# Kernel optimization log

Measured on AMD Instinct MI355X. Metric: run time of the kernel, lower is better.

## Reference

```python
import jax, jax.numpy as jnp
import numpy as np

VEC_DIM = 64
RANK = 2


def setup_inputs() -> dict:
    key = jax.random.key(0)
    kg, km, kp = jax.random.split(key, 3)
    grid = jax.random.normal(kg, (193, 193, VEC_DIM), dtype=jnp.float32)
    # nn.init.uniform_(M.weight, -0.5, 0.5)
    M_weight = jax.random.uniform(km, (VEC_DIM, VEC_DIM), minval=-0.5, maxval=0.5, dtype=jnp.float32)
    # nn.init.uniform_(P, -0.1, 0.1)
    P = jax.random.uniform(kp, (VEC_DIM, VEC_DIM), minval=-0.1, maxval=0.1, dtype=jnp.float32)
    return {"grid": grid, "M_weight": M_weight, "P": P}


def reference(grid, M_weight, P):
    H, W, m = grid.shape
    # periods1[i,j] = periods2[i,j] = i*m + j + 2
    periods = (jnp.arange(m, dtype=jnp.float32)[:, None] * m
               + jnp.arange(m, dtype=jnp.float32)[None, :] + 2.0)  # [m, m]

    # ---- window extraction: linear mode (step=1), rank_mode='drop', rank_op='avg' ----
    nH = H - RANK + 1
    nW = W - RANK + 1
    win_sum = jax.lax.reduce_window(grid, 0.0, jax.lax.add,
                                    (RANK, RANK, 1), (1, 1, 1), 'VALID')  # [nH, nW, m]
    x_win = (win_sum / float(RANK * RANK)).reshape(nH * nW, m)  # [B, m]

    # ---- map through M (nn.Linear, no bias): y = x @ W^T ----
    x = x_win @ M_weight.T  # [B, m]

    # ---- phi_table gather: phi[k1,k2] = cos(2*pi*k1/periods) * cos(2*pi*k2/periods) ----
    two_pi = jnp.float32(2.0 * np.pi)
    k1s = jnp.arange(nH, dtype=jnp.float32)
    k2s = jnp.arange(nW, dtype=jnp.float32)
    cos1 = jnp.cos(two_pi * k1s[:, None, None] / periods)  # [nH, m, m]
    cos2 = jnp.cos(two_pi * k2s[:, None, None] / periods)  # [nW, m, m]
    phi = (cos1[:, None, :, :] * cos2[None, :, :, :]).reshape(nH * nW, m, m)  # [B, m, m]

    # ---- Nk = einsum('bj,ij,bij->bi', x, P, phi) ----
    Nk = jnp.einsum('bj,ij,bij->bi', x, P, phi)  # [B, m]
    return Nk
```

## Files before the change

### kernel.cpp

```cpp
#include <hip/hip_runtime.h>
#include <math.h>

#define NH 192
#define NW 192
#define Wt 193
#define TG 24
#define NTILE (TG*TG)
#define TILE_SZ 4096
#define TBLK 3072

__device__ __forceinline__ float cos_rev(float num, float den) {
    float rev = num * __builtin_amdgcn_rcpf(den);
    rev = __builtin_amdgcn_fractf(rev);
    return __builtin_amdgcn_cosf(rev);
}

__global__ __launch_bounds__(256) void k_prep(const float* __restrict__ grid,
                                              const float* __restrict__ Mw,
                                              const float* __restrict__ P,
                                              float* __restrict__ Cz,
                                              float* __restrict__ CP1,
                                              float* __restrict__ xt) {
    __shared__ float Ms[64 * 64];
    __shared__ float win[64 * 68];
    int bx = blockIdx.x;
    int t = threadIdx.x;

    if (bx < TBLK) {
        int idx = bx * 256 + t;
        int r  = idx & 3;
        int i  = (idx >> 2) & 63;
        int kg = (idx >> 8) % 48;
        int j  = idx / 12288;
        int k  = kg * 4 + r;
        Cz[idx] = cos_rev((float)k, (float)(i * 64 + j + 2));
        int i2 = idx & 63;
        int k2 = (idx >> 6) % 192;
        int j2 = idx / 12288;
        int t2 = i2 * 64 + j2;
        CP1[idx] = cos_rev((float)k2, (float)(t2 + 2)) * P[t2];
        return;
    }

    int bb = bx - TBLK;
    int k1g = bb % TG, k2g = bb / TG;

    #pragma unroll
    for (int r = 0; r < 4; ++r) {
        int e = r * 256 + t;
        ((float4*)Ms)[e] = ((const float4*)Mw)[e];
    }

    {
        int c = t & 63, pq = t >> 6;
        const float* gb = grid + ((size_t)(k1g * 8) * Wt + k2g * 8) * 64;
        #pragma unroll
        for (int r = 0; r < 16; ++r) {
            int p = pq * 16 + r;
            int l1 = p >> 3, l2 = p & 7;
            const float* g0 = gb + ((size_t)l1 * Wt + l2) * 64;
            float s = g0[c] + g0[64 + c] + g0[Wt * 64 + c] + g0[Wt * 64 + 64 + c];
            win[p * 68 + c] = 0.25f * s;
        }
    }
    __syncthreads();

    int p = t & 63, jq = t >> 6;
    float4 wv[16];
    #pragma unroll
    for (int q = 0; q < 16; ++q) wv[q] = *(const float4*)&win[p * 68 + 4 * q];

    float* xb = xt + (size_t)(k1g * TG + k2g) * TILE_SZ;
    #pragma unroll
    for (int r = 0; r < 16; ++r) {
        int j = jq * 16 + r;
        float acc = 0.f;
        #pragma unroll
        for (int q = 0; q < 16; ++q) {
            float4 mv = *(const float4*)&Ms[j * 64 + 4 * q];
            acc += wv[q].x * mv.x + wv[q].y * mv.y + wv[q].z * mv.z + wv[q].w * mv.w;
        }
        xb[(size_t)j * 64 + p] = acc;
    }
}

__global__ __launch_bounds__(512) void k_main(const float* __restrict__ xt,
                                              const float* __restrict__ Cz,
                                              const float* __restrict__ CP1,
                                              float* __restrict__ out) {
    __shared__ float4 cs[2048];
    int bx = blockIdx.x;
    int k1g = bx % TG, k2g = bx / TG;
    int t = threadIdx.x;
    int lane = t & 63;
    int w = __builtin_amdgcn_readfirstlane(t >> 6);
    int k1 = k1g * 8 + w;

    const float*  c1p = CP1 + (size_t)k1 * 64 + lane;
    const float*  xb  = xt + (size_t)(k1g * TG + k2g) * TILE_SZ + w * 8;
    const float4* Cz4 = (const float4*)Cz;
    int kgb = k2g * 2;

    float acc[8];
    #pragma unroll
    for (int l2 = 0; l2 < 8; ++l2) acc[l2] = 0.f;

    for (int jc = 0; jc < 4; ++jc) {
        __syncthreads();
        #pragma unroll
        for (int r = 0; r < 4; ++r) {
            int e = r * 512 + t;
            int jj = e >> 7;
            int g  = (e >> 6) & 1;
            int i  = e & 63;
            cs[e] = Cz4[(size_t)((jc * 16 + jj) * 48 + kgb + g) * 64 + i];
        }
        __syncthreads();

        #pragma unroll 4
        for (int jj = 0; jj < 16; ++jj) {
            int j = jc * 16 + jj;
            float  c1 = c1p[(size_t)j * 12288];
            float4 v0 = cs[jj * 128 + lane];
            float4 v1 = cs[jj * 128 + 64 + lane];
            const float4* xj = (const float4*)(xb + (size_t)j * 64);
            float4 x0 = xj[0];
            float4 x1 = xj[1];
            float c2f[8] = {v0.x, v0.y, v0.z, v0.w, v1.x, v1.y, v1.z, v1.w};
            float xs[8]  = {x0.x, x0.y, x0.z, x0.w, x1.x, x1.y, x1.z, x1.w};
            #pragma unroll
            for (int l2 = 0; l2 < 8; ++l2)
                acc[l2] += xs[l2] * (c1 * c2f[l2]);
        }
    }

    size_t ob = ((size_t)k1 * NW + k2g * 8) * 64 + lane;
    #pragma unroll
    for (int l2 = 0; l2 < 8; ++l2)
        out[ob + (size_t)l2 * 64] = acc[l2];
}

extern "C" void kernel_launch(void* const* d_in, const int* in_sizes, int n_in,
                              void* d_out, int out_size, void* d_ws, size_t ws_size,
                              hipStream_t stream) {
    const float* grid = (const float*)d_in[0];
    const float* Mw   = (const float*)d_in[1];
    const float* P    = (const float*)d_in[2];
    float* out = (float*)d_out;

    float* Cz  = (float*)d_ws;
    float* CP1 = Cz + 786432;
    float* xt  = CP1 + 786432;

    k_prep<<<TBLK + NTILE, 256, 0, stream>>>(grid, Mw, P, Cz, CP1, xt);
    k_main<<<NTILE, 512, 0, stream>>>(xt, Cz, CP1, out);
}
```

Before: 94.97 us.

## Fuse window-average and M projection into main contraction kernel

Splits the cosine-table generation into its own 512-thread kernel and moves the per-tile window averaging plus M-weight projection into the main contraction kernel. Each block computes its x tile, writes it to workspace, and reads it back after a barrier. Shared memory is reused between the Ms/win buffers and the cosine staging buffer. This removes one kernel boundary and lets the projection and contraction of a tile run back to back in one block. In exchange, the table generation no longer overlaps with the projection work, and the fused kernel now holds more registers per thread.

```diff
diff --git a/kernel.cpp b/kernel.cpp
--- a/kernel.cpp
+++ b/kernel.cpp
@@ -7,7 +7,7 @@
 #define TG 24
 #define NTILE (TG*TG)
 #define TILE_SZ 4096
-#define TBLK 3072
+#define TBLK 1536
 
 __device__ __forceinline__ float cos_rev(float num, float den) {
     float rev = num * __builtin_amdgcn_rcpf(den);
@@ -15,48 +15,49 @@
     return __builtin_amdgcn_cosf(rev);
 }
 
-__global__ __launch_bounds__(256) void k_prep(const float* __restrict__ grid,
-                                              const float* __restrict__ Mw,
-                                              const float* __restrict__ P,
-                                              float* __restrict__ Cz,
-                                              float* __restrict__ CP1,
-                                              float* __restrict__ xt) {
-    __shared__ float Ms[64 * 64];
-    __shared__ float win[64 * 68];
+__global__ __launch_bounds__(512) void k_tables(const float* __restrict__ P,
+                                                float* __restrict__ Cz,
+                                                float* __restrict__ CP1) {
+    int idx = blockIdx.x * 512 + threadIdx.x;
+    int r  = idx & 3;
+    int i  = (idx >> 2) & 63;
+    int kg = (idx >> 8) % 48;
+    int j  = idx / 12288;
+    int k  = kg * 4 + r;
+    Cz[idx] = cos_rev((float)k, (float)(i * 64 + j + 2));
+    int i2 = idx & 63;
+    int k2 = (idx >> 6) % 192;
+    int j2 = idx / 12288;
+    int t2 = i2 * 64 + j2;
+    CP1[idx] = cos_rev((float)k2, (float)(t2 + 2)) * P[t2];
+}
+
+__global__ __launch_bounds__(512) void k_fused(const float* __restrict__ grid,
+                                               const float* __restrict__ Mw,
+                                               const float* __restrict__ Cz,
+                                               const float* __restrict__ CP1,
+                                               float* __restrict__ xt,
+                                               float* __restrict__ out) {
+    __shared__ __align__(16) float smem[8448];
+    float* Ms  = smem;
+    float* win = smem + 4096;
+    float4* cs = (float4*)smem;
+
     int bx = blockIdx.x;
+    int k1g = bx % TG, k2g = bx / TG;
     int t = threadIdx.x;
 
-    if (bx < TBLK) {
-        int idx = bx * 256 + t;
-        int r  = idx & 3;
-        int i  = (idx >> 2) & 63;
-        int kg = (idx >> 8) % 48;
-        int j  = idx / 12288;
-        int k  = kg * 4 + r;
-        Cz[idx] = cos_rev((float)k, (float)(i * 64 + j + 2));
-        int i2 = idx & 63;
-        int k2 = (idx >> 6) % 192;
-        int j2 = idx / 12288;
-        int t2 = i2 * 64 + j2;
-        CP1[idx] = cos_rev((float)k2, (float)(t2 + 2)) * P[t2];
-        return;
-    }
-
-    int bb = bx - TBLK;
-    int k1g = bb % TG, k2g = bb / TG;
-
     #pragma unroll
-    for (int r = 0; r < 4; ++r) {
-        int e = r * 256 + t;
+    for (int r = 0; r < 2; ++r) {
+        int e = r * 512 + t;
         ((float4*)Ms)[e] = ((const float4*)Mw)[e];
     }
-
     {
         int c = t & 63, pq = t >> 6;
         const float* gb = grid + ((size_t)(k1g * 8) * Wt + k2g * 8) * 64;
         #pragma unroll
-        for (int r = 0; r < 16; ++r) {
-            int p = pq * 16 + r;
+        for (int r = 0; r < 8; ++r) {
+            int p = pq * 8 + r;
             int l1 = p >> 3, l2 = p & 7;
             const float* g0 = gb + ((size_t)l1 * Wt + l2) * 64;
             float s = g0[c] + g0[64 + c] + g0[Wt * 64 + c] + g0[Wt * 64 + 64 + c];
@@ -65,39 +66,32 @@
     }
     __syncthreads();
 
-    int p = t & 63, jq = t >> 6;
-    float4 wv[16];
-    #pragma unroll
-    for (int q = 0; q < 16; ++q) wv[q] = *(const float4*)&win[p * 68 + 4 * q];
+    {
+        int p = t & 63, jq = t >> 6;
+        float4 wv[16];
+        #pragma unroll
+        for (int q = 0; q < 16; ++q) wv[q] = *(const float4*)&win[p * 68 + 4 * q];
 
-    float* xb = xt + (size_t)(k1g * TG + k2g) * TILE_SZ;
-    #pragma unroll
-    for (int r = 0; r < 16; ++r) {
-        int j = jq * 16 + r;
-        float acc = 0.f;
+        float* xb = xt + (size_t)(k1g * TG + k2g) * TILE_SZ;
         #pragma unroll
-        for (int q = 0; q < 16; ++q) {
-            float4 mv = *(const float4*)&Ms[j * 64 + 4 * q];
-            acc += wv[q].x * mv.x + wv[q].y * mv.y + wv[q].z * mv.z + wv[q].w * mv.w;
+        for (int r = 0; r < 8; ++r) {
+            int j = jq * 8 + r;
+            float acc = 0.f;
+            #pragma unroll
+            for (int q = 0; q < 16; ++q) {
+                float4 mv = *(const float4*)&Ms[j * 64 + 4 * q];
+                acc += wv[q].x * mv.x + wv[q].y * mv.y + wv[q].z * mv.z + wv[q].w * mv.w;
+            }
+            xb[(size_t)j * 64 + p] = acc;
         }
-        xb[(size_t)j * 64 + p] = acc;
     }
-}
 
-__global__ __launch_bounds__(512) void k_main(const float* __restrict__ xt,
-                                              const float* __restrict__ Cz,
-                                              const float* __restrict__ CP1,
-                                              float* __restrict__ out) {
-    __shared__ float4 cs[2048];
-    int bx = blockIdx.x;
-    int k1g = bx % TG, k2g = bx / TG;
-    int t = threadIdx.x;
     int lane = t & 63;
     int w = __builtin_amdgcn_readfirstlane(t >> 6);
     int k1 = k1g * 8 + w;
 
     const float*  c1p = CP1 + (size_t)k1 * 64 + lane;
-    const float*  xb  = xt + (size_t)(k1g * TG + k2g) * TILE_SZ + w * 8;
+    const float*  xb2 = xt + (size_t)(k1g * TG + k2g) * TILE_SZ + w * 8;
     const float4* Cz4 = (const float4*)Cz;
     int kgb = k2g * 2;
 
@@ -123,7 +117,7 @@
             float  c1 = c1p[(size_t)j * 12288];
             float4 v0 = cs[jj * 128 + lane];
             float4 v1 = cs[jj * 128 + 64 + lane];
-            const float4* xj = (const float4*)(xb + (size_t)j * 64);
+            const float4* xj = (const float4*)(xb2 + (size_t)j * 64);
             float4 x0 = xj[0];
             float4 x1 = xj[1];
             float c2f[8] = {v0.x, v0.y, v0.z, v0.w, v1.x, v1.y, v1.z, v1.w};
@@ -134,7 +128,7 @@
         }
     }
 
-    size_t ob = ((size_t)k1 * NW + k2g * 8) * 64 + lane;
+    size_t ob = ((size_t)k1 * NW + kgb * 4) * 64 + lane;
     #pragma unroll
     for (int l2 = 0; l2 < 8; ++l2)
         out[ob + (size_t)l2 * 64] = acc[l2];
@@ -152,6 +146,6 @@
     float* CP1 = Cz + 786432;
     float* xt  = CP1 + 786432;
 
-    k_prep<<<TBLK + NTILE, 256, 0, stream>>>(grid, Mw, P, Cz, CP1, xt);
-    k_main<<<NTILE, 512, 0, stream>>>(xt, Cz, CP1, out);
+    k_tables<<<TBLK, 512, 0, stream>>>(P, Cz, CP1);
+    k_fused<<<NTILE, 512, 0, stream>>>(grid, Mw, Cz, CP1, xt, out);
 }
```

Result: slower. 106.3 us (+11.9%).
